# Optimization experiments

Hardware: AMD Instinct MI355X
Metric: run time of the kernel (lower is better)

Reference implementation:

```python
import jax, jax.numpy as jnp
import numpy as np

N = 100000   # nodes
E = 1600000  # edges
IN = 128     # in_dim
C = 32       # hidden_dim
H = 2        # heads1
G = 64       # graphs in batch
NEG_SLOPE = 0.2


def setup_inputs() -> dict:
    key = jax.random.key(0)
    ks = jax.random.split(key, 20)
    f = lambda k, shape: jax.random.normal(k, shape, dtype=jnp.float32) * 0.05
    return {
        "x": jax.random.normal(ks[0], (N, IN), dtype=jnp.float32),
        "edge_index": jax.random.randint(ks[1], (2, E), 0, N, dtype=jnp.int32),
        "batch": jnp.sort(jax.random.randint(ks[2], (N,), 0, G, dtype=jnp.int32)),
        # GATv2 layer 1: lin_l / lin_r [IN, H*C], att [H, C], bias [H*C]
        "Wl1": f(ks[3], (IN, H * C)), "Wr1": f(ks[4], (IN, H * C)),
        "att1": f(ks[5], (H, C)), "b1": f(ks[6], (H * C,)),
        # GATv2 layer 2: heads=1
        "Wl2": f(ks[7], (H * C, C)), "Wr2": f(ks[8], (H * C, C)),
        "att2": f(ks[9], (1, C)), "b2": f(ks[10], (C,)),
        # GlobalAttention gate_nn: Linear(C,C) -> ReLU -> Linear(C,1)
        "g1w": f(ks[11], (C, C)), "g1b": f(ks[12], (C,)),
        "g2w": f(ks[13], (C, 1)), "g2b": f(ks[14], (1,)),
        # MLP head
        "lin1w": f(ks[15], (C, C)), "lin1b": f(ks[16], (C,)),
        "lin2w": f(ks[17], (C, 1)), "lin2b": f(ks[18], (1,)),
    }


def _gatv2(x, src, dst, Wl, Wr, att, bias, heads, ch):
    """PyG GATv2Conv (concat=True, share_weights=False, eval mode)."""
    n = x.shape[0]
    xl = (x @ Wl).reshape(n, heads, ch)  # source transform (also the message)
    xr = (x @ Wr).reshape(n, heads, ch)  # target transform
    e = jax.nn.leaky_relu(xl[src] + xr[dst], negative_slope=NEG_SLOPE)  # [E,H,C]
    score = jnp.einsum('ehc,hc->eh', e, att)  # [E,H]
    # scatter-softmax over incoming edges of each destination node
    m = jax.ops.segment_max(score, dst, num_segments=n)
    m = jnp.where(jnp.isfinite(m), m, 0.0)  # nodes w/o in-edges
    ex = jnp.exp(score - m[dst])
    denom = jax.ops.segment_sum(ex, dst, num_segments=n)
    alpha = ex / denom[dst]  # [E,H]
    out = jax.ops.segment_sum(alpha[:, :, None] * xl[src], dst, num_segments=n)
    return out.reshape(n, heads * ch) + bias


def reference(x, edge_index, batch, Wl1, Wr1, att1, b1, Wl2, Wr2, att2, b2,
              g1w, g1b, g2w, g2b, lin1w, lin1b, lin2w, lin2b):
    src, dst = edge_index[0], edge_index[1]
    h = jax.nn.relu(_gatv2(x, src, dst, Wl1, Wr1, att1, b1, H, C))   # [N, H*C]
    h = jax.nn.relu(_gatv2(h, src, dst, Wl2, Wr2, att2, b2, 1, C))   # [N, C]
    # GlobalAttention pooling: softmax(gate_nn(h)) over nodes of each graph
    gate = jax.nn.relu(h @ g1w + g1b) @ g2w + g2b                     # [N,1]
    gm = jax.ops.segment_max(gate, batch, num_segments=G)
    gm = jnp.where(jnp.isfinite(gm), gm, 0.0)
    ge = jnp.exp(gate - gm[batch])
    gd = jax.ops.segment_sum(ge, batch, num_segments=G)
    attw = ge / gd[batch]                                             # [N,1]
    pooled = jax.ops.segment_sum(attw * h, batch, num_segments=G)     # [G,C]
    z = jax.nn.relu(pooled @ lin1w + lin1b)
    return (z @ lin2w + lin2b).squeeze(-1)                            # [G]
```

## Files before the change

kernel.cpp:

```cpp
#include <hip/hip_runtime.h>
#include <hip/hip_fp16.h>
#include <cfloat>
#include <cstdint>
#include <cstddef>

#define N_NODES 100000
#define N_EDGES 1600000
#define G_GRAPHS 64
#define BKT_SHIFT 9
#define BKT_NODES (1 << BKT_SHIFT)
#define NBKT ((N_NODES + BKT_NODES - 1) >> BKT_SHIFT)
#define BKT_STRIDE 12288
#define SRC_BITS 17

typedef _Float16 hvec2 __attribute__((ext_vector_type(2)));
typedef _Float16 hvec4 __attribute__((ext_vector_type(4)));
typedef _Float16 hvec8 __attribute__((ext_vector_type(8)));
typedef float f32x4 __attribute__((ext_vector_type(4)));

#define LOG2E 1.4426950408889634f

static __device__ __forceinline__ float fdot2(hvec2 a, hvec2 b, float c) {
#if __has_builtin(__builtin_amdgcn_fdot2)
  return __builtin_amdgcn_fdot2(a, b, c, false);
#else
  return fmaf((float)a.y, (float)b.y, fmaf((float)a.x, (float)b.x, c));
#endif
}

static __device__ __forceinline__ hvec2 leaky2(hvec2 v) {
  return __builtin_elementwise_max(v, v * (_Float16)0.2f);
}

static __device__ __forceinline__ float fast_exp2(float x) {
#if __has_builtin(__builtin_amdgcn_exp2f)
  return __builtin_amdgcn_exp2f(x);
#else
  return exp2f(x);
#endif
}

template <int CTRL>
static __device__ __forceinline__ float dppadd(float v) {
  const int vi = __builtin_bit_cast(int, v);
  const int ti = __builtin_amdgcn_update_dpp(0, vi, CTRL, 0xF, 0xF, true);
  return v + __builtin_bit_cast(float, ti);
}
static __device__ __forceinline__ float dpp_sum8(float v) {
  v = dppadd<0xB1>(v);
  v = dppadd<0x4E>(v);
  v = dppadd<0x141>(v);
  return v;
}

__launch_bounds__(1024) __global__
void partA_kernel(const int* __restrict__ ei, int* __restrict__ bcursor,
                  int* __restrict__ staging,
                  const float* __restrict__ Wl1, const float* __restrict__ Wr1,
                  const float* __restrict__ Wl2, const float* __restrict__ Wr2,
                  __half* __restrict__ Wh1, __half* __restrict__ Wh2) {
  const int tid = threadIdx.x;
  const int widx = blockIdx.x * 1024 + tid;
  if (widx < 2 * 128 * 64) {
    const int j2 = widx / 128;
    const int k = widx - j2 * 128;
    const int j = (j2 < 64) ? j2 : j2 - 64;
    Wh1[widx] =
        __float2half((j2 < 64) ? Wl1[k * 64 + j] : Wr1[k * 64 + j]);
  } else if (widx < 2 * 128 * 64 + 2 * 64 * 32) {
    const int i2 = widx - 2 * 128 * 64;
    const int j2 = i2 / 64;
    const int k = i2 - j2 * 64;
    const int j = (j2 < 32) ? j2 : j2 - 32;
    Wh2[i2] = __float2half((j2 < 32) ? Wl2[k * 32 + j] : Wr2[k * 32 + j]);
  }

  __shared__ int lh[NBKT];
  __shared__ int lbase[NBKT];
  for (int i = tid; i < NBKT; i += 1024) lh[i] = 0;
  __syncthreads();
  const int e0 = blockIdx.x * 4096 + tid;
  int pk[4], b[4];
#pragma unroll
  for (int k = 0; k < 4; ++k) {
    const int e = e0 + k * 1024;
    const bool ok = e < N_EDGES;
    const int s = ok ? ei[e] : 0;
    const int d = ok ? ei[N_EDGES + e] : 0;
    pk[k] = s | ((d & (BKT_NODES - 1)) << SRC_BITS);
    b[k] = ok ? (d >> BKT_SHIFT) : -1;
    if (ok) atomicAdd(&lh[b[k]], 1);
  }
  __syncthreads();
  for (int i = tid; i < NBKT; i += 1024) {
    const int c = lh[i];
    lbase[i] = i * BKT_STRIDE + (c ? atomicAdd(&bcursor[i], c) : 0);
    lh[i] = 0;
  }
  __syncthreads();
#pragma unroll
  for (int k = 0; k < 4; ++k) {
    if (b[k] >= 0) {
      const int p = lbase[b[k]] + atomicAdd(&lh[b[k]], 1);
      staging[p] = pk[k];
    }
  }
}

#define GEMM1_K 128
#define GEMM1_J 64
#define SMEM_BYTES (64 * (GEMM1_K + 8) * 2 + 2 * GEMM1_J * (GEMM1_K + 8) * 2)

__launch_bounds__(256) __global__
void partB_gemm1_kernel(const int* __restrict__ staging,
                        const int* __restrict__ bcursor,
                        int2* __restrict__ rowdeg, int* __restrict__ csr_src,
                        const float* __restrict__ A,
                        const __half* __restrict__ Wh,
                        __half* __restrict__ O0, __half* __restrict__ O1) {
  __shared__ __align__(16) char smem[SMEM_BYTES];
  const int tid = threadIdx.x;

  if (blockIdx.x < NBKT) {
    int* ldeg = (int*)smem;
    int* lsc = (int*)(smem + BKT_NODES * 4);
    const int b = blockIdx.x;
    const int node0 = b << BKT_SHIFT;
    const int start = b * BKT_STRIDE;
    const int cnt = bcursor[b];
    if (tid < 64) csr_src[start + cnt + tid] = 0;
    ldeg[2 * tid] = 0;
    ldeg[2 * tid + 1] = 0;
    __syncthreads();
    for (int i = tid; i < cnt; i += 256)
      atomicAdd(&ldeg[staging[start + i] >> SRC_BITS], 1);
    __syncthreads();
    const int d0 = ldeg[2 * tid];
    const int d1 = ldeg[2 * tid + 1];
    const int psum = d0 + d1;
    lsc[tid] = psum;
    __syncthreads();
    for (int d = 1; d < 256; d <<= 1) {
      const int t = (tid >= d) ? lsc[tid - d] : 0;
      __syncthreads();
      lsc[tid] += t;
      __syncthreads();
    }
    const int ex = lsc[tid] - psum + start;
    const int n0 = node0 + 2 * tid;
    if (n0 < N_NODES)
      *reinterpret_cast<int4*>(&rowdeg[n0]) = make_int4(ex, d0, ex + d0, d1);
    __syncthreads();
    ldeg[2 * tid] = ex;
    ldeg[2 * tid + 1] = ex + d0;
    __syncthreads();
    for (int i = tid; i < cnt; i += 256) {
      const int pk = staging[start + i];
      const int p = atomicAdd(&ldeg[pk >> SRC_BITS], 1);
      csr_src[p] = pk & ((1 << SRC_BITS) - 1);
    }
    return;
  }

  constexpr int K = GEMM1_K;
  constexpr int J = GEMM1_J;
  constexpr int KP = K + 8;
  constexpr int J2 = 2 * J;
  typedef __half(*AldsT)[KP];
  AldsT Alds = (AldsT)smem;
  AldsT Wlds = (AldsT)(smem + 64 * KP * 2);
  const int n0 = (blockIdx.x - NBKT) * 64;

  for (int c = tid; c < J2 * (K / 8); c += 256) {
    const int j = c / (K / 8);
    const int k8 = c - j * (K / 8);
    const uint4 w = reinterpret_cast<const uint4*>(Wh)[c];
    *reinterpret_cast<uint4*>(&Wlds[j][k8 * 8]) = w;
  }
  for (int c = tid; c < 64 * (K / 4); c += 256) {
    const int r = c / (K / 4);
    const int k4 = c - r * (K / 4);
    const int row = n0 + r;
    float4 v = make_float4(0.f, 0.f, 0.f, 0.f);
    if (row < N_NODES)
      v = reinterpret_cast<const float4*>(A)[(size_t)row * (K / 4) + k4];
    const hvec4 h = {(_Float16)v.x, (_Float16)v.y, (_Float16)v.z,
                     (_Float16)v.w};
    *reinterpret_cast<hvec4*>(&Alds[r][k4 * 4]) = h;
  }
  __syncthreads();

  const int wv = tid >> 6;
  const int l = tid & 63;
  const int lr = l & 15;
  const int lk = l >> 4;

  hvec8 afrag[K / 32];
#pragma unroll
  for (int kc = 0; kc < K / 32; ++kc)
    afrag[kc] = *reinterpret_cast<const hvec8*>(
        &Alds[wv * 16 + lr][kc * 32 + 8 * lk]);

#pragma unroll
  for (int jt = 0; jt < J2 / 16; ++jt) {
    f32x4 acc = {0.f, 0.f, 0.f, 0.f};
#pragma unroll
    for (int kc = 0; kc < K / 32; ++kc) {
      const hvec8 b = *reinterpret_cast<const hvec8*>(
          &Wlds[jt * 16 + lr][kc * 32 + 8 * lk]);
      acc = __builtin_amdgcn_mfma_f32_16x16x32_f16(afrag[kc], b, acc, 0, 0, 0);
    }
    const int colt = jt * 16 + lr;
    const int rowb = n0 + wv * 16 + 4 * lk;
#pragma unroll
    for (int r = 0; r < 4; ++r) {
      const int row = rowb + r;
      if (row < N_NODES) {
        if (jt < J / 16)
          O0[(size_t)row * J + colt] = __float2half(acc[r]);
        else
          O1[(size_t)row * J + (colt - J)] = __float2half(acc[r]);
      }
    }
  }
}

template <int K, int J>
__launch_bounds__(256) __global__
void gemm_mfma2(const __half* __restrict__ Ah, const __half* __restrict__ Wh,
                const float* __restrict__ bias, __half* __restrict__ O0,
                __half* __restrict__ O1) {
  constexpr int KP = K + 8;
  constexpr int J2 = 2 * J;
  __shared__ __align__(16) __half Alds[64][KP];
  __shared__ __align__(16) __half Wlds[J2][KP];
  const int tid = threadIdx.x;
  const int n0 = blockIdx.x * 64;

  for (int c = tid; c < J2 * (K / 8); c += 256) {
    const int j = c / (K / 8);
    const int k8 = c - j * (K / 8);
    const uint4 w = reinterpret_cast<const uint4*>(Wh)[c];
    *reinterpret_cast<uint4*>(&Wlds[j][k8 * 8]) = w;
  }
  for (int c = tid; c < 64 * (K / 4); c += 256) {
    const int r = c / (K / 4);
    const int k4 = c - r * (K / 4);
    const int row = n0 + r;
    hvec4 h = {(_Float16)0.f, (_Float16)0.f, (_Float16)0.f, (_Float16)0.f};
    if (row < N_NODES) {
      const hvec4 a =
          *reinterpret_cast<const hvec4*>(Ah + (size_t)row * K + 4 * k4);
      const float4 b = reinterpret_cast<const float4*>(bias)[k4];
      h.x = (_Float16)fmaxf((float)a.x + b.x, 0.f);
      h.y = (_Float16)fmaxf((float)a.y + b.y, 0.f);
      h.z = (_Float16)fmaxf((float)a.z + b.z, 0.f);
      h.w = (_Float16)fmaxf((float)a.w + b.w, 0.f);
    }
    *reinterpret_cast<hvec4*>(&Alds[r][k4 * 4]) = h;
  }
  __syncthreads();

  const int wv = tid >> 6;
  const int l = tid & 63;
  const int lr = l & 15;
  const int lk = l >> 4;

  hvec8 afrag[K / 32];
#pragma unroll
  for (int kc = 0; kc < K / 32; ++kc)
    afrag[kc] = *reinterpret_cast<const hvec8*>(
        &Alds[wv * 16 + lr][kc * 32 + 8 * lk]);

#pragma unroll
  for (int jt = 0; jt < J2 / 16; ++jt) {
    f32x4 acc = {0.f, 0.f, 0.f, 0.f};
#pragma unroll
    for (int kc = 0; kc < K / 32; ++kc) {
      const hvec8 b = *reinterpret_cast<const hvec8*>(
          &Wlds[jt * 16 + lr][kc * 32 + 8 * lk]);
      acc = __builtin_amdgcn_mfma_f32_16x16x32_f16(afrag[kc], b, acc, 0, 0, 0);
    }
    const int colt = jt * 16 + lr;
    const int rowb = n0 + wv * 16 + 4 * lk;
#pragma unroll
    for (int r = 0; r < 4; ++r) {
      const int row = rowb + r;
      if (row < N_NODES) {
        if (jt < J / 16)
          O0[(size_t)row * J + colt] = __float2half(acc[r]);
        else
          O1[(size_t)row * J + (colt - J)] = __float2half(acc[r]);
      }
    }
  }
}

__launch_bounds__(256) __global__
void gat1_kernel(const __half* __restrict__ xlh, const __half* __restrict__ xrh,
                 const float* __restrict__ att, const int2* __restrict__ rowdeg,
                 const int* __restrict__ csr_src, __half* __restrict__ aggh) {
  const int n =
      __builtin_amdgcn_readfirstlane(blockIdx.x * 4 + (threadIdx.x >> 6));
  if (n >= N_NODES) return;
  const int lane = threadIdx.x & 63;
  const int g = lane >> 4;
  const int m = lane & 15;
  const int2 rd = rowdeg[n];
  const int r0 = __builtin_amdgcn_readfirstlane(rd.x);
  const int dg = __builtin_amdgcn_readfirstlane(rd.y);

  const hvec4 xrv =
      *reinterpret_cast<const hvec4*>(xrh + ((size_t)n << 6) + 4 * m);
  const hvec2 xh01 = {xrv.x, xrv.y};
  const hvec2 xh23 = {xrv.z, xrv.w};
  const float4 atf = *reinterpret_cast<const float4*>(att + 4 * m);
  const hvec2 at01 = {(_Float16)(atf.x * LOG2E), (_Float16)(atf.y * LOG2E)};
  const hvec2 at23 = {(_Float16)(atf.z * LOG2E), (_Float16)(atf.w * LOG2E)};

  float s = 0.f, acc0 = 0.f, acc1 = 0.f, acc2 = 0.f, acc3 = 0.f;

  auto gather1 = [&](int sel) -> uint2 {
    return *reinterpret_cast<const uint2*>(
        (const char*)xlh + (((size_t)(unsigned)sel) << 7) + 8 * m);
  };
  auto compute1 = [&](int q, uint2 buf, int rem) {
    const hvec2 a01 = __builtin_bit_cast(hvec2, buf.x);
    const hvec2 a23 = __builtin_bit_cast(hvec2, buf.y);
    const hvec2 v01 = leaky2(a01 + xh01);
    const hvec2 v23 = leaky2(a23 + xh23);
    float p = fdot2(v23, at23, fdot2(v01, at01, 0.f));
    p = dpp_sum8(p);
    float e = fast_exp2(p);
    e = (4 * q + g < rem) ? e : 0.f;
    s += e;
    acc0 = fmaf(e, (float)a01.x, acc0);
    acc1 = fmaf(e, (float)a01.y, acc1);
    acc2 = fmaf(e, (float)a23.x, acc2);
    acc3 = fmaf(e, (float)a23.y, acc3);
  };

  for (int c0 = 0; c0 < dg; c0 += 64) {
    const int rem = dg - c0;
    const int* cp = csr_src + r0 + c0 + (lane >> 4);
    const int Kc = (min(rem, 64) + 3) >> 2;
#pragma unroll
    for (int g0 = 0; g0 < 16; g0 += 4) {
      if (g0 < Kc) {
        int sq[4];
#pragma unroll
        for (int k = 0; k < 4; ++k) sq[k] = cp[4 * (g0 + k)];
        uint2 B[4];
#pragma unroll
        for (int k = 0; k < 4; ++k)
          if (g0 + k < Kc) B[k] = gather1(sq[k]);
#pragma unroll
        for (int k = 0; k < 4; ++k)
          if (g0 + k < Kc) compute1(g0 + k, B[k], rem);
      }
    }
  }

  s += __shfl_xor(s, 16);
  s += __shfl_xor(s, 32);
  acc0 += __shfl_xor(acc0, 16);
  acc0 += __shfl_xor(acc0, 32);
  acc1 += __shfl_xor(acc1, 16);
  acc1 += __shfl_xor(acc1, 32);
  acc2 += __shfl_xor(acc2, 16);
  acc2 += __shfl_xor(acc2, 32);
  acc3 += __shfl_xor(acc3, 16);
  acc3 += __shfl_xor(acc3, 32);
  const float inv = s > 0.f ? 1.f / s : 0.f;
  if (g == 0) {
    const hvec4 o = {(_Float16)(acc0 * inv), (_Float16)(acc1 * inv),
                     (_Float16)(acc2 * inv), (_Float16)(acc3 * inv)};
    *reinterpret_cast<hvec4*>(aggh + ((size_t)n << 6) + 4 * m) = o;
  }
}

__launch_bounds__(256) __global__
void gat2_kernel(const __half* __restrict__ xlh, const __half* __restrict__ xrh,
                 const float* __restrict__ att, const int2* __restrict__ rowdeg,
                 const int* __restrict__ csr_src, const float* __restrict__ b2,
                 float* __restrict__ h2) {
  const int n =
      __builtin_amdgcn_readfirstlane(blockIdx.x * 4 + (threadIdx.x >> 6));
  if (n >= N_NODES) return;
  const int lane = threadIdx.x & 63;
  const int g = lane >> 3;
  const int m = lane & 7;
  const int2 rd = rowdeg[n];
  const int r0 = __builtin_amdgcn_readfirstlane(rd.x);
  const int dg = __builtin_amdgcn_readfirstlane(rd.y);

  const hvec4 xrv =
      *reinterpret_cast<const hvec4*>(xrh + (size_t)n * 32 + 4 * m);
  const hvec2 xh01 = {xrv.x, xrv.y};
  const hvec2 xh23 = {xrv.z, xrv.w};
  const float4 atf = *reinterpret_cast<const float4*>(att + 4 * m);
  const hvec2 at01 = {(_Float16)(atf.x * LOG2E), (_Float16)(atf.y * LOG2E)};
  const hvec2 at23 = {(_Float16)(atf.z * LOG2E), (_Float16)(atf.w * LOG2E)};

  float s = 0.f, acc0 = 0.f, acc1 = 0.f, acc2 = 0.f, acc3 = 0.f;

  auto gather1 = [&](int sel) -> uint2 {
    return *reinterpret_cast<const uint2*>(
        (const char*)xlh + (((size_t)(unsigned)sel) << 6) + 8 * m);
  };
  auto compute1 = [&](int q, uint2 buf, int rem) {
    const hvec2 a01 = __builtin_bit_cast(hvec2, buf.x);
    const hvec2 a23 = __builtin_bit_cast(hvec2, buf.y);
    const hvec2 v01 = leaky2(a01 + xh01);
    const hvec2 v23 = leaky2(a23 + xh23);
    float p = fdot2(v23, at23, fdot2(v01, at01, 0.f));
    p = dpp_sum8(p);
    float e = fast_exp2(p);
    e = (8 * q + g < rem) ? e : 0.f;
    s += e;
    acc0 = fmaf(e, (float)a01.x, acc0);
    acc1 = fmaf(e, (float)a01.y, acc1);
    acc2 = fmaf(e, (float)a23.x, acc2);
    acc3 = fmaf(e, (float)a23.y, acc3);
  };

  for (int c0 = 0; c0 < dg; c0 += 64) {
    const int rem = dg - c0;
    const int* cp = csr_src + r0 + c0 + (lane >> 3);
    const int Kc = (min(rem, 64) + 7) >> 3;
#pragma unroll
    for (int g0 = 0; g0 < 8; g0 += 4) {
      if (g0 < Kc) {
        int sq[4];
#pragma unroll
        for (int k = 0; k < 4; ++k) sq[k] = cp[8 * (g0 + k)];
        uint2 B[4];
#pragma unroll
        for (int k = 0; k < 4; ++k)
          if (g0 + k < Kc) B[k] = gather1(sq[k]);
#pragma unroll
        for (int k = 0; k < 4; ++k)
          if (g0 + k < Kc) compute1(g0 + k, B[k], rem);
      }
    }
  }

  s += __shfl_xor(s, 8);
  s += __shfl_xor(s, 16);
  s += __shfl_xor(s, 32);
  acc0 += __shfl_xor(acc0, 8);
  acc0 += __shfl_xor(acc0, 16);
  acc0 += __shfl_xor(acc0, 32);
  acc1 += __shfl_xor(acc1, 8);
  acc1 += __shfl_xor(acc1, 16);
  acc1 += __shfl_xor(acc1, 32);
  acc2 += __shfl_xor(acc2, 8);
  acc2 += __shfl_xor(acc2, 16);
  acc2 += __shfl_xor(acc2, 32);
  acc3 += __shfl_xor(acc3, 8);
  acc3 += __shfl_xor(acc3, 16);
  acc3 += __shfl_xor(acc3, 32);
  const float inv = s > 0.f ? 1.f / s : 0.f;
  const float4 b2v = *reinterpret_cast<const float4*>(b2 + 4 * m);
  if (g == 0)
    *reinterpret_cast<float4*>(h2 + (size_t)n * 32 + 4 * m) =
        make_float4(fmaxf(fmaf(acc0, inv, b2v.x), 0.f),
                    fmaxf(fmaf(acc1, inv, b2v.y), 0.f),
                    fmaxf(fmaf(acc2, inv, b2v.z), 0.f),
                    fmaxf(fmaf(acc3, inv, b2v.w), 0.f));
}

__launch_bounds__(256) __global__
void gepool_kernel(const float* __restrict__ h2, const int* __restrict__ batch,
                   const float* __restrict__ g1w, const float* __restrict__ g1b,
                   const float* __restrict__ g2w, const float* __restrict__ g2b,
                   float* __restrict__ gd, float* __restrict__ pooled) {
  __shared__ float Wg[32 * 32];
  __shared__ float Hs[128][32];
  __shared__ float pool[G_GRAPHS * 32];
  __shared__ float gdb[G_GRAPHS];
  const int tid = threadIdx.x;
  for (int i = tid; i < 1024; i += 256) Wg[i] = g1w[i];
  for (int i = tid; i < G_GRAPHS * 32; i += 256) pool[i] = 0.f;
  if (tid < G_GRAPHS) gdb[tid] = 0.f;
  const int start = blockIdx.x * 128;
  for (int i = tid; i < 128 * 8; i += 256) {
    const int n = start + (i >> 3);
    const int q = i & 7;
    float4 v = make_float4(0.f, 0.f, 0.f, 0.f);
    if (n < N_NODES)
      v = reinterpret_cast<const float4*>(h2)[(size_t)n * 8 + q];
    *reinterpret_cast<float4*>(&Hs[i >> 3][q * 4]) = v;
  }
  __syncthreads();
  const int c = tid & 31;
  const int slot = tid >> 5;
  const float g1bc = g1b[c];
  const float g2wc = g2w[c];
  const float g2b0 = g2b[0];
  for (int ln = slot; ln < 128; ln += 8) {
    const int n = start + ln;
    if (n >= N_NODES) break;
    float sg = g1bc;
#pragma unroll
    for (int k4 = 0; k4 < 8; ++k4) {
      const float4 hq = *reinterpret_cast<const float4*>(&Hs[ln][4 * k4]);
      sg = fmaf(hq.x, Wg[(4 * k4 + 0) * 32 + c], sg);
      sg = fmaf(hq.y, Wg[(4 * k4 + 1) * 32 + c], sg);
      sg = fmaf(hq.z, Wg[(4 * k4 + 2) * 32 + c], sg);
      sg = fmaf(hq.w, Wg[(4 * k4 + 3) * 32 + c], sg);
    }
    sg = fmaxf(sg, 0.f);
    float pg = sg * g2wc;
    pg += __shfl_xor(pg, 1);
    pg += __shfl_xor(pg, 2);
    pg += __shfl_xor(pg, 4);
    pg += __shfl_xor(pg, 8);
    pg += __shfl_xor(pg, 16);
    const float ge = __expf(pg + g2b0);
    const int b = batch[n];
    atomicAdd(&pool[b * 32 + c], ge * Hs[ln][c]);
    if (c == 0) atomicAdd(&gdb[b], ge);
  }
  __syncthreads();
  for (int i = tid; i < G_GRAPHS * 32; i += 256)
    if (pool[i] != 0.f) unsafeAtomicAdd(&pooled[i], pool[i]);
  if (tid < G_GRAPHS && gdb[tid] != 0.f) unsafeAtomicAdd(&gd[tid], gdb[tid]);
}

__launch_bounds__(64) __global__
void final_kernel(const float* __restrict__ pooled, const float* __restrict__ gd,
                  const float* __restrict__ l1w, const float* __restrict__ l1b,
                  const float* __restrict__ l2w, const float* __restrict__ l2b,
                  float* __restrict__ out) {
  const int g = blockIdx.x;
  const int lane = threadIdx.x;
  if (lane >= 32) return;
  const float invgd = 1.f / gd[g];
  float s = l1b[lane];
#pragma unroll
  for (int k = 0; k < 32; ++k)
    s = fmaf(pooled[g * 32 + k] * invgd, l1w[k * 32 + lane], s);
  s = fmaxf(s, 0.f);
  float p = s * l2w[lane];
  p += __shfl_xor(p, 1);
  p += __shfl_xor(p, 2);
  p += __shfl_xor(p, 4);
  p += __shfl_xor(p, 8);
  p += __shfl_xor(p, 16);
  if (lane == 0) out[g] = p + l2b[0];
}

extern "C" void kernel_launch(void* const* d_in, const int* in_sizes, int n_in,
                              void* d_out, int out_size, void* d_ws,
                              size_t ws_size, hipStream_t stream) {
  const float* x    = (const float*)d_in[0];
  const int*   ei   = (const int*)d_in[1];
  const int*   batch= (const int*)d_in[2];
  const float* Wl1  = (const float*)d_in[3];
  const float* Wr1  = (const float*)d_in[4];
  const float* att1 = (const float*)d_in[5];
  const float* b1   = (const float*)d_in[6];
  const float* Wl2  = (const float*)d_in[7];
  const float* Wr2  = (const float*)d_in[8];
  const float* att2 = (const float*)d_in[9];
  const float* b2   = (const float*)d_in[10];
  const float* g1w  = (const float*)d_in[11];
  const float* g1b  = (const float*)d_in[12];
  const float* g2w  = (const float*)d_in[13];
  const float* g2b  = (const float*)d_in[14];
  const float* l1w  = (const float*)d_in[15];
  const float* l1b  = (const float*)d_in[16];
  const float* l2w  = (const float*)d_in[17];
  const float* l2b  = (const float*)d_in[18];
  float* out = (float*)d_out;

  int* zbase = (int*)d_ws;
  int* bcursor = zbase;
  float* gd = (float*)(zbase + 256);
  float* pooled = gd + G_GRAPHS;
  int2* rowdeg = (int2*)(pooled + G_GRAPHS * 32);
  int* csr_src = (int*)(rowdeg + N_NODES);
  int* staging = csr_src + (size_t)NBKT * BKT_STRIDE;
  __half* xr1h = (__half*)(staging + (size_t)NBKT * BKT_STRIDE);
  __half* agg1h = xr1h + (size_t)N_NODES * 64;
  __half* Wh1 = agg1h + (size_t)N_NODES * 64;
  __half* Wh2 = Wh1 + 128 * 128;
  __half* xl1h = Wh2 + 64 * 64;
  float* h2 = (float*)(xl1h + (size_t)N_NODES * 64);
  __half* xl2h = xl1h;
  __half* xr2h = xr1h;

  (void)hipMemsetAsync(zbase, 0, (size_t)(256 + 64 + 2048) * sizeof(int),
                       stream);

  partA_kernel<<<(N_EDGES + 4095) / 4096, 1024, 0, stream>>>(
      ei, bcursor, staging, Wl1, Wr1, Wl2, Wr2, Wh1, Wh2);

  partB_gemm1_kernel<<<NBKT + (N_NODES + 63) / 64, 256, 0, stream>>>(
      staging, bcursor, rowdeg, csr_src, x, Wh1, xl1h, xr1h);

  gat1_kernel<<<(N_NODES + 3) / 4, 256, 0, stream>>>(xl1h, xr1h, att1, rowdeg,
                                                     csr_src, agg1h);

  gemm_mfma2<64, 32><<<(N_NODES + 63) / 64, 256, 0, stream>>>(agg1h, Wh2, b1,
                                                              xl2h, xr2h);
  gat2_kernel<<<(N_NODES + 3) / 4, 256, 0, stream>>>(xl2h, xr2h, att2, rowdeg,
                                                     csr_src, b2, h2);

  gepool_kernel<<<(N_NODES + 127) / 128, 256, 0, stream>>>(
      h2, batch, g1w, g1b, g2w, g2b, gd, pooled);
  final_kernel<<<64, 64, 0, stream>>>(pooled, gd, l1w, l1b, l2w, l2b, out);
}
```

Baseline: 302.0 us.

## Make GAT aggregation kernels persistent with next-node prefetch across iterations

Each wave in the two GATv2 aggregation kernels now handles 4 nodes, strided by 25000, instead of one. While it computes the current node's gathers, it prefetches the next node's rowdeg, xr row and first CSR source indices. This is meant to hide the serial load chain (rowdeg, then csr, then gather) at the start of each node and to cut wave launch overhead. In exchange it raises register pressure, lowers the number of waves in flight, and hardcodes N=100000 as 4x25000.

```diff
diff --git a/kernel.cpp b/kernel.cpp
--- a/kernel.cpp
+++ b/kernel.cpp
@@ -12,6 +12,8 @@
 #define NBKT ((N_NODES + BKT_NODES - 1) >> BKT_SHIFT)
 #define BKT_STRIDE 12288
 #define SRC_BITS 17
+#define GAT_WAVES 25000
+#define GAT_NITER 4
 
 typedef _Float16 hvec2 __attribute__((ext_vector_type(2)));
 typedef _Float16 hvec4 __attribute__((ext_vector_type(4)));
@@ -300,82 +302,140 @@
 void gat1_kernel(const __half* __restrict__ xlh, const __half* __restrict__ xrh,
                  const float* __restrict__ att, const int2* __restrict__ rowdeg,
                  const int* __restrict__ csr_src, __half* __restrict__ aggh) {
-  const int n =
-      __builtin_amdgcn_readfirstlane(blockIdx.x * 4 + (threadIdx.x >> 6));
-  if (n >= N_NODES) return;
+  const int wid = blockIdx.x * 4 + (threadIdx.x >> 6);
+  if (wid >= GAT_WAVES) return;
   const int lane = threadIdx.x & 63;
   const int g = lane >> 4;
   const int m = lane & 15;
-  const int2 rd = rowdeg[n];
-  const int r0 = __builtin_amdgcn_readfirstlane(rd.x);
-  const int dg = __builtin_amdgcn_readfirstlane(rd.y);
-
-  const hvec4 xrv =
-      *reinterpret_cast<const hvec4*>(xrh + ((size_t)n << 6) + 4 * m);
-  const hvec2 xh01 = {xrv.x, xrv.y};
-  const hvec2 xh23 = {xrv.z, xrv.w};
   const float4 atf = *reinterpret_cast<const float4*>(att + 4 * m);
   const hvec2 at01 = {(_Float16)(atf.x * LOG2E), (_Float16)(atf.y * LOG2E)};
   const hvec2 at23 = {(_Float16)(atf.z * LOG2E), (_Float16)(atf.w * LOG2E)};
-
-  float s = 0.f, acc0 = 0.f, acc1 = 0.f, acc2 = 0.f, acc3 = 0.f;
 
   auto gather1 = [&](int sel) -> uint2 {
     return *reinterpret_cast<const uint2*>(
         (const char*)xlh + (((size_t)(unsigned)sel) << 7) + 8 * m);
   };
-  auto compute1 = [&](int q, uint2 buf, int rem) {
-    const hvec2 a01 = __builtin_bit_cast(hvec2, buf.x);
-    const hvec2 a23 = __builtin_bit_cast(hvec2, buf.y);
-    const hvec2 v01 = leaky2(a01 + xh01);
-    const hvec2 v23 = leaky2(a23 + xh23);
-    float p = fdot2(v23, at23, fdot2(v01, at01, 0.f));
-    p = dpp_sum8(p);
-    float e = fast_exp2(p);
-    e = (4 * q + g < rem) ? e : 0.f;
-    s += e;
-    acc0 = fmaf(e, (float)a01.x, acc0);
-    acc1 = fmaf(e, (float)a01.y, acc1);
-    acc2 = fmaf(e, (float)a23.x, acc2);
-    acc3 = fmaf(e, (float)a23.y, acc3);
-  };
-
-  for (int c0 = 0; c0 < dg; c0 += 64) {
-    const int rem = dg - c0;
-    const int* cp = csr_src + r0 + c0 + (lane >> 4);
+
+  int n = wid;
+  int2 rd = rowdeg[n];
+  hvec4 xrv = *reinterpret_cast<const hvec4*>(xrh + ((size_t)n << 6) + 4 * m);
+  int r0 = __builtin_amdgcn_readfirstlane(rd.x);
+  int dgc = __builtin_amdgcn_readfirstlane(rd.y);
+  int sq0[4];
+  {
+    const int* cp = csr_src + r0 + g;
+#pragma unroll
+    for (int k = 0; k < 4; ++k) sq0[k] = cp[4 * k];
+  }
+
+#pragma unroll
+  for (int it = 0; it < GAT_NITER; ++it) {
+    const int rem = dgc;
     const int Kc = (min(rem, 64) + 3) >> 2;
-#pragma unroll
-    for (int g0 = 0; g0 < 16; g0 += 4) {
-      if (g0 < Kc) {
-        int sq[4];
-#pragma unroll
-        for (int k = 0; k < 4; ++k) sq[k] = cp[4 * (g0 + k)];
-        uint2 B[4];
-#pragma unroll
-        for (int k = 0; k < 4; ++k)
-          if (g0 + k < Kc) B[k] = gather1(sq[k]);
-#pragma unroll
-        for (int k = 0; k < 4; ++k)
-          if (g0 + k < Kc) compute1(g0 + k, B[k], rem);
+    uint2 B0[4];
+#pragma unroll
+    for (int k = 0; k < 4; ++k)
+      if (k < Kc) B0[k] = gather1(sq0[k]);
+
+    int2 rd_n = rd;
+    hvec4 xr_n = xrv;
+    int r0_n = r0, dg_n = dgc;
+    int sq0_n[4] = {0, 0, 0, 0};
+    if (it + 1 < GAT_NITER) {
+      const int nn = n + GAT_WAVES;
+      rd_n = rowdeg[nn];
+      xr_n = *reinterpret_cast<const hvec4*>(xrh + ((size_t)nn << 6) + 4 * m);
+      r0_n = __builtin_amdgcn_readfirstlane(rd_n.x);
+      dg_n = __builtin_amdgcn_readfirstlane(rd_n.y);
+      const int* cpn = csr_src + r0_n + g;
+#pragma unroll
+      for (int k = 0; k < 4; ++k) sq0_n[k] = cpn[4 * k];
+    }
+
+    const hvec2 xh01 = {xrv.x, xrv.y};
+    const hvec2 xh23 = {xrv.z, xrv.w};
+    float s = 0.f, acc0 = 0.f, acc1 = 0.f, acc2 = 0.f, acc3 = 0.f;
+    auto compute1 = [&](int q, uint2 buf, int rm) {
+      const hvec2 a01 = __builtin_bit_cast(hvec2, buf.x);
+      const hvec2 a23 = __builtin_bit_cast(hvec2, buf.y);
+      const hvec2 v01 = leaky2(a01 + xh01);
+      const hvec2 v23 = leaky2(a23 + xh23);
+      float p = fdot2(v23, at23, fdot2(v01, at01, 0.f));
+      p = dpp_sum8(p);
+      float e = fast_exp2(p);
+      e = (4 * q + g < rm) ? e : 0.f;
+      s += e;
+      acc0 = fmaf(e, (float)a01.x, acc0);
+      acc1 = fmaf(e, (float)a01.y, acc1);
+      acc2 = fmaf(e, (float)a23.x, acc2);
+      acc3 = fmaf(e, (float)a23.y, acc3);
+    };
+#pragma unroll
+    for (int k = 0; k < 4; ++k)
+      if (k < Kc) compute1(k, B0[k], rem);
+    {
+      const int* cp = csr_src + r0 + g;
+#pragma unroll
+      for (int g0 = 4; g0 < 16; g0 += 4) {
+        if (g0 < Kc) {
+          int sq[4];
+#pragma unroll
+          for (int k = 0; k < 4; ++k) sq[k] = cp[4 * (g0 + k)];
+          uint2 B[4];
+#pragma unroll
+          for (int k = 0; k < 4; ++k)
+            if (g0 + k < Kc) B[k] = gather1(sq[k]);
+#pragma unroll
+          for (int k = 0; k < 4; ++k)
+            if (g0 + k < Kc) compute1(g0 + k, B[k], rem);
+        }
       }
     }
-  }
-
-  s += __shfl_xor(s, 16);
-  s += __shfl_xor(s, 32);
-  acc0 += __shfl_xor(acc0, 16);
-  acc0 += __shfl_xor(acc0, 32);
-  acc1 += __shfl_xor(acc1, 16);
-  acc1 += __shfl_xor(acc1, 32);
-  acc2 += __shfl_xor(acc2, 16);
-  acc2 += __shfl_xor(acc2, 32);
-  acc3 += __shfl_xor(acc3, 16);
-  acc3 += __shfl_xor(acc3, 32);
-  const float inv = s > 0.f ? 1.f / s : 0.f;
-  if (g == 0) {
-    const hvec4 o = {(_Float16)(acc0 * inv), (_Float16)(acc1 * inv),
-                     (_Float16)(acc2 * inv), (_Float16)(acc3 * inv)};
-    *reinterpret_cast<hvec4*>(aggh + ((size_t)n << 6) + 4 * m) = o;
+    for (int c0 = 64; c0 < dgc; c0 += 64) {
+      const int rem2 = dgc - c0;
+      const int* cp = csr_src + r0 + c0 + g;
+      const int Kc2 = (min(rem2, 64) + 3) >> 2;
+#pragma unroll
+      for (int g0 = 0; g0 < 16; g0 += 4) {
+        if (g0 < Kc2) {
+          int sq[4];
+#pragma unroll
+          for (int k = 0; k < 4; ++k) sq[k] = cp[4 * (g0 + k)];
+          uint2 B[4];
+#pragma unroll
+          for (int k = 0; k < 4; ++k)
+            if (g0 + k < Kc2) B[k] = gather1(sq[k]);
+#pragma unroll
+          for (int k = 0; k < 4; ++k)
+            if (g0 + k < Kc2) compute1(g0 + k, B[k], rem2);
+        }
+      }
+    }
+
+    s += __shfl_xor(s, 16);
+    s += __shfl_xor(s, 32);
+    acc0 += __shfl_xor(acc0, 16);
+    acc0 += __shfl_xor(acc0, 32);
+    acc1 += __shfl_xor(acc1, 16);
+    acc1 += __shfl_xor(acc1, 32);
+    acc2 += __shfl_xor(acc2, 16);
+    acc2 += __shfl_xor(acc2, 32);
+    acc3 += __shfl_xor(acc3, 16);
+    acc3 += __shfl_xor(acc3, 32);
+    const float inv = s > 0.f ? 1.f / s : 0.f;
+    if (g == 0) {
+      const hvec4 o = {(_Float16)(acc0 * inv), (_Float16)(acc1 * inv),
+                       (_Float16)(acc2 * inv), (_Float16)(acc3 * inv)};
+      *reinterpret_cast<hvec4*>(aggh + ((size_t)n << 6) + 4 * m) = o;
+    }
+
+    n += GAT_WAVES;
+    rd = rd_n;
+    xrv = xr_n;
+    r0 = r0_n;
+    dgc = dg_n;
+#pragma unroll
+    for (int k = 0; k < 4; ++k) sq0[k] = sq0_n[k];
   }
 }
 
@@ -384,90 +444,145 @@
                  const float* __restrict__ att, const int2* __restrict__ rowdeg,
                  const int* __restrict__ csr_src, const float* __restrict__ b2,
                  float* __restrict__ h2) {
-  const int n =
-      __builtin_amdgcn_readfirstlane(blockIdx.x * 4 + (threadIdx.x >> 6));
-  if (n >= N_NODES) return;
+  const int wid = blockIdx.x * 4 + (threadIdx.x >> 6);
+  if (wid >= GAT_WAVES) return;
   const int lane = threadIdx.x & 63;
   const int g = lane >> 3;
   const int m = lane & 7;
-  const int2 rd = rowdeg[n];
-  const int r0 = __builtin_amdgcn_readfirstlane(rd.x);
-  const int dg = __builtin_amdgcn_readfirstlane(rd.y);
-
-  const hvec4 xrv =
-      *reinterpret_cast<const hvec4*>(xrh + (size_t)n * 32 + 4 * m);
-  const hvec2 xh01 = {xrv.x, xrv.y};
-  const hvec2 xh23 = {xrv.z, xrv.w};
   const float4 atf = *reinterpret_cast<const float4*>(att + 4 * m);
   const hvec2 at01 = {(_Float16)(atf.x * LOG2E), (_Float16)(atf.y * LOG2E)};
   const hvec2 at23 = {(_Float16)(atf.z * LOG2E), (_Float16)(atf.w * LOG2E)};
-
-  float s = 0.f, acc0 = 0.f, acc1 = 0.f, acc2 = 0.f, acc3 = 0.f;
+  const float4 b2v = *reinterpret_cast<const float4*>(b2 + 4 * m);
 
   auto gather1 = [&](int sel) -> uint2 {
     return *reinterpret_cast<const uint2*>(
         (const char*)xlh + (((size_t)(unsigned)sel) << 6) + 8 * m);
   };
-  auto compute1 = [&](int q, uint2 buf, int rem) {
-    const hvec2 a01 = __builtin_bit_cast(hvec2, buf.x);
-    const hvec2 a23 = __builtin_bit_cast(hvec2, buf.y);
-    const hvec2 v01 = leaky2(a01 + xh01);
-    const hvec2 v23 = leaky2(a23 + xh23);
-    float p = fdot2(v23, at23, fdot2(v01, at01, 0.f));
-    p = dpp_sum8(p);
-    float e = fast_exp2(p);
-    e = (8 * q + g < rem) ? e : 0.f;
-    s += e;
-    acc0 = fmaf(e, (float)a01.x, acc0);
-    acc1 = fmaf(e, (float)a01.y, acc1);
-    acc2 = fmaf(e, (float)a23.x, acc2);
-    acc3 = fmaf(e, (float)a23.y, acc3);
-  };
-
-  for (int c0 = 0; c0 < dg; c0 += 64) {
-    const int rem = dg - c0;
-    const int* cp = csr_src + r0 + c0 + (lane >> 3);
+
+  int n = wid;
+  int2 rd = rowdeg[n];
+  hvec4 xrv = *reinterpret_cast<const hvec4*>(xrh + (size_t)n * 32 + 4 * m);
+  int r0 = __builtin_amdgcn_readfirstlane(rd.x);
+  int dgc = __builtin_amdgcn_readfirstlane(rd.y);
+  int sq0[4];
+  {
+    const int* cp = csr_src + r0 + g;
+#pragma unroll
+    for (int k = 0; k < 4; ++k) sq0[k] = cp[8 * k];
+  }
+
+#pragma unroll
+  for (int it = 0; it < GAT_NITER; ++it) {
+    const int rem = dgc;
     const int Kc = (min(rem, 64) + 7) >> 3;
-#pragma unroll
-    for (int g0 = 0; g0 < 8; g0 += 4) {
-      if (g0 < Kc) {
+    uint2 B0[4];
+#pragma unroll
+    for (int k = 0; k < 4; ++k)
+      if (k < Kc) B0[k] = gather1(sq0[k]);
+
+    int2 rd_n = rd;
+    hvec4 xr_n = xrv;
+    int r0_n = r0, dg_n = dgc;
+    int sq0_n[4] = {0, 0, 0, 0};
+    if (it + 1 < GAT_NITER) {
+      const int nn = n + GAT_WAVES;
+      rd_n = rowdeg[nn];
+      xr_n = *reinterpret_cast<const hvec4*>(xrh + (size_t)nn * 32 + 4 * m);
+      r0_n = __builtin_amdgcn_readfirstlane(rd_n.x);
+      dg_n = __builtin_amdgcn_readfirstlane(rd_n.y);
+      const int* cpn = csr_src + r0_n + g;
+#pragma unroll
+      for (int k = 0; k < 4; ++k) sq0_n[k] = cpn[8 * k];
+    }
+
+    const hvec2 xh01 = {xrv.x, xrv.y};
+    const hvec2 xh23 = {xrv.z, xrv.w};
+    float s = 0.f, acc0 = 0.f, acc1 = 0.f, acc2 = 0.f, acc3 = 0.f;
+    auto compute1 = [&](int q, uint2 buf, int rm) {
+      const hvec2 a01 = __builtin_bit_cast(hvec2, buf.x);
+      const hvec2 a23 = __builtin_bit_cast(hvec2, buf.y);
+      const hvec2 v01 = leaky2(a01 + xh01);
+      const hvec2 v23 = leaky2(a23 + xh23);
+      float p = fdot2(v23, at23, fdot2(v01, at01, 0.f));
+      p = dpp_sum8(p);
+      float e = fast_exp2(p);
+      e = (8 * q + g < rm) ? e : 0.f;
+      s += e;
+      acc0 = fmaf(e, (float)a01.x, acc0);
+      acc1 = fmaf(e, (float)a01.y, acc1);
+      acc2 = fmaf(e, (float)a23.x, acc2);
+      acc3 = fmaf(e, (float)a23.y, acc3);
+    };
+#pragma unroll
+    for (int k = 0; k < 4; ++k)
+      if (k < Kc) compute1(k, B0[k], rem);
+    {
+      const int* cp = csr_src + r0 + g;
+      if (4 < Kc) {
         int sq[4];
 #pragma unroll
-        for (int k = 0; k < 4; ++k) sq[k] = cp[8 * (g0 + k)];
+        for (int k = 0; k < 4; ++k) sq[k] = cp[8 * (4 + k)];
         uint2 B[4];
 #pragma unroll
         for (int k = 0; k < 4; ++k)
-          if (g0 + k < Kc) B[k] = gather1(sq[k]);
+          if (4 + k < Kc) B[k] = gather1(sq[k]);
 #pragma unroll
         for (int k = 0; k < 4; ++k)
-          if (g0 + k < Kc) compute1(g0 + k, B[k], rem);
+          if (4 + k < Kc) compute1(4 + k, B[k], rem);
       }
     }
-  }
-
-  s += __shfl_xor(s, 8);
-  s += __shfl_xor(s, 16);
-  s += __shfl_xor(s, 32);
-  acc0 += __shfl_xor(acc0, 8);
-  acc0 += __shfl_xor(acc0, 16);
-  acc0 += __shfl_xor(acc0, 32);
-  acc1 += __shfl_xor(acc1, 8);
-  acc1 += __shfl_xor(acc1, 16);
-  acc1 += __shfl_xor(acc1, 32);
-  acc2 += __shfl_xor(acc2, 8);
-  acc2 += __shfl_xor(acc2, 16);
-  acc2 += __shfl_xor(acc2, 32);
-  acc3 += __shfl_xor(acc3, 8);
-  acc3 += __shfl_xor(acc3, 16);
-  acc3 += __shfl_xor(acc3, 32);
-  const float inv = s > 0.f ? 1.f / s : 0.f;
-  const float4 b2v = *reinterpret_cast<const float4*>(b2 + 4 * m);
-  if (g == 0)
-    *reinterpret_cast<float4*>(h2 + (size_t)n * 32 + 4 * m) =
-        make_float4(fmaxf(fmaf(acc0, inv, b2v.x), 0.f),
-                    fmaxf(fmaf(acc1, inv, b2v.y), 0.f),
-                    fmaxf(fmaf(acc2, inv, b2v.z), 0.f),
-                    fmaxf(fmaf(acc3, inv, b2v.w), 0.f));
+    for (int c0 = 64; c0 < dgc; c0 += 64) {
+      const int rem2 = dgc - c0;
+      const int* cp = csr_src + r0 + c0 + g;
+      const int Kc2 = (min(rem2, 64) + 7) >> 3;
+#pragma unroll
+      for (int g0 = 0; g0 < 8; g0 += 4) {
+        if (g0 < Kc2) {
+          int sq[4];
+#pragma unroll
+          for (int k = 0; k < 4; ++k) sq[k] = cp[8 * (g0 + k)];
+          uint2 B[4];
+#pragma unroll
+          for (int k = 0; k < 4; ++k)
+            if (g0 + k < Kc2) B[k] = gather1(sq[k]);
+#pragma unroll
+          for (int k = 0; k < 4; ++k)
+            if (g0 + k < Kc2) compute1(g0 + k, B[k], rem2);
+        }
+      }
+    }
+
+    s += __shfl_xor(s, 8);
+    s += __shfl_xor(s, 16);
+    s += __shfl_xor(s, 32);
+    acc0 += __shfl_xor(acc0, 8);
+    acc0 += __shfl_xor(acc0, 16);
+    acc0 += __shfl_xor(acc0, 32);
+    acc1 += __shfl_xor(acc1, 8);
+    acc1 += __shfl_xor(acc1, 16);
+    acc1 += __shfl_xor(acc1, 32);
+    acc2 += __shfl_xor(acc2, 8);
+    acc2 += __shfl_xor(acc2, 16);
+    acc2 += __shfl_xor(acc2, 32);
+    acc3 += __shfl_xor(acc3, 8);
+    acc3 += __shfl_xor(acc3, 16);
+    acc3 += __shfl_xor(acc3, 32);
+    const float inv = s > 0.f ? 1.f / s : 0.f;
+    if (g == 0)
+      *reinterpret_cast<float4*>(h2 + (size_t)n * 32 + 4 * m) =
+          make_float4(fmaxf(fmaf(acc0, inv, b2v.x), 0.f),
+                      fmaxf(fmaf(acc1, inv, b2v.y), 0.f),
+                      fmaxf(fmaf(acc2, inv, b2v.z), 0.f),
+                      fmaxf(fmaf(acc3, inv, b2v.w), 0.f));
+
+    n += GAT_WAVES;
+    rd = rd_n;
+    xrv = xr_n;
+    r0 = r0_n;
+    dgc = dg_n;
+#pragma unroll
+    for (int k = 0; k < 4; ++k) sq0[k] = sq0_n[k];
+  }
 }
 
 __launch_bounds__(256) __global__
@@ -600,13 +715,13 @@
   partB_gemm1_kernel<<<NBKT + (N_NODES + 63) / 64, 256, 0, stream>>>(
       staging, bcursor, rowdeg, csr_src, x, Wh1, xl1h, xr1h);
 
-  gat1_kernel<<<(N_NODES + 3) / 4, 256, 0, stream>>>(xl1h, xr1h, att1, rowdeg,
-                                                     csr_src, agg1h);
+  gat1_kernel<<<(GAT_WAVES + 3) / 4, 256, 0, stream>>>(xl1h, xr1h, att1,
+                                                       rowdeg, csr_src, agg1h);
 
   gemm_mfma2<64, 32><<<(N_NODES + 63) / 64, 256, 0, stream>>>(agg1h, Wh2, b1,
                                                               xl2h, xr2h);
-  gat2_kernel<<<(N_NODES + 3) / 4, 256, 0, stream>>>(xl2h, xr2h, att2, rowdeg,
-                                                     csr_src, b2, h2);
+  gat2_kernel<<<(GAT_WAVES + 3) / 4, 256, 0, stream>>>(xl2h, xr2h, att2,
+                                                       rowdeg, csr_src, b2, h2);
 
   gepool_kernel<<<(N_NODES + 127) / 128, 256, 0, stream>>>(
       h2, batch, g1w, g1b, g2w, g2b, gd, pooled);
```

Result: no change. 305.4 us (+1.1%).
